# Kernel tuning notes

Hardware: AMD Instinct MI355X
Metric: run time of the kernel (lower is better)

The kernel has to match this reference:

```python
import jax, jax.numpy as jnp
import numpy as np

B, C, H, W = 16, 32, 240, 240  # C=32 forced: C//2 must equal 16 pooled-query tokens
CH = C // 2


def conv1x1(x, Wt, bt):
    # 1x1 conv == per-pixel matmul over channels
    return jnp.einsum('bchw,oc->bohw', x, Wt) + bt[None, :, None, None]


def adaptive_pool6(x):
    # AdaptiveAvgPool2d((6,6)) with H,W divisible by 6 -> uniform block mean
    b, c, h, w = x.shape
    return x.reshape(b, c, 6, h // 6, 6, w // 6).mean(axis=(3, 5))


def setup_inputs() -> dict:
    key = jax.random.key(0)
    ks = jax.random.split(key, 24)
    wsc, bsc = 0.05, 0.01
    def wmat(k, o, i):
        return jax.random.normal(k, (o, i), jnp.float32) * wsc
    def bvec(k, o):
        return jax.random.normal(k, (o,), jnp.float32) * bsc
    inp = {
        'x1': jax.random.normal(ks[0], (B, C, H, W), jnp.float32),
        'x2': jax.random.normal(ks[1], (B, C, H, W), jnp.float32),
        'Wq1': wmat(ks[2], CH, C), 'bq1': bvec(ks[3], CH),
        'Wk1': wmat(ks[4], CH, C), 'bk1': bvec(ks[5], CH),
        'Wv1': wmat(ks[6], CH, C), 'bv1': bvec(ks[7], CH),
        'Wq2': wmat(ks[8], CH, C), 'bq2': bvec(ks[9], CH),
        'Wk2': wmat(ks[10], CH, C), 'bk2': bvec(ks[11], CH),
        'Wv2': wmat(ks[12], CH, C), 'bv2': bvec(ks[13], CH),
        'Wc1': wmat(ks[14], C, CH), 'bc1': bvec(ks[15], C),
        'Wc2': wmat(ks[16], C, CH), 'bc2': bvec(ks[17], C),
        # module inits gammas to 0; use small nonzero so the attention path affects output
        'gamma1': jnp.float32(0.1),
        'gamma2': jnp.float32(0.1),
    }
    return inp


def reference(x1, x2, Wq1, bq1, Wk1, bk1, Wv1, bv1, Wq2, bq2, Wk2, bk2,
              Wv2, bv2, Wc1, bc1, Wc2, bc2, gamma1, gamma2):
    b, c, h, w = x1.shape
    hw = h * w
    ch = c // 2
    # pooled queries: 6x6 adaptive pool, crop interior 4x4 -> 16 tokens
    q1 = adaptive_pool6(conv1x1(x1, Wq1, bq1))[:, :, 1:-1, 1:-1]
    q1 = q1.reshape(b, ch, 16).transpose(0, 2, 1)          # [B,16,ch]
    k1 = conv1x1(x1, Wk1, bk1).reshape(b, ch, hw)           # [B,ch,HW]
    v1 = conv1x1(x1, Wv1, bv1).reshape(b, ch, hw)
    q2 = adaptive_pool6(conv1x1(x2, Wq2, bq2))[:, :, 1:-1, 1:-1]
    q2 = q2.reshape(b, ch, 16).transpose(0, 2, 1)
    k2 = conv1x1(x2, Wk2, bk2).reshape(b, ch, hw)
    v2 = conv1x1(x2, Wv2, bv2).reshape(b, ch, hw)

    attn2 = jax.nn.softmax(jnp.einsum('bqc,bcn->bqn', q1, k2), axis=-1)  # [B,16,HW]
    out1 = (v1 * attn2).reshape(b, ch, h, w)   # elementwise (ch == 16)
    out1 = conv1x1(out1, Wc2, bc2)

    attn1 = jax.nn.softmax(jnp.einsum('bqc,bcn->bqn', q2, k1), axis=-1)
    out2 = (v2 * attn1).reshape(b, ch, h, w)
    out2 = conv1x1(out2, Wc1, bc1)

    return (x1 + gamma1 * out1, x2 + gamma2 * out2)
```

## Files before the change

kernel.cpp:

```cpp
#include <hip/hip_runtime.h>

#define HW 57600
#define BATCH 16

#define L_OFF    0
#define AT_OFF   512
#define CV_OFF   16896
#define XM_OFF   17408
#define WVT_OFF  33792

__global__ void k1a_pool(const float* __restrict__ x1, const float* __restrict__ x2,
                         float* __restrict__ ws) {
  int task = blockIdx.x * 4 + (threadIdx.x >> 6);
  int lane = threadIdx.x & 63;
  int t = task & 15, i = (task >> 4) & 31, b = (task >> 9) & 15, s = task >> 13;
  int bi = 1 + (t >> 2), bj = 1 + (t & 3);
  const float* xp = (s ? x2 : x1) + (size_t)(b * 32 + i) * HW + (40 * bi) * 240 + 40 * bj;
  float sum = 0.f;
  #pragma unroll
  for (int k = 0; k < 25; ++k) {
    int e = lane + 64 * k;
    int r = e / 40, c = e - r * 40;
    sum += xp[r * 240 + c];
  }
  #pragma unroll
  for (int off = 32; off; off >>= 1) sum += __shfl_down(sum, off);
  if (lane == 0) ws[XM_OFF + task] = sum * (1.0f / 1600.0f);
}

__global__ void k1b_fold(float* __restrict__ ws,
                         const float* __restrict__ Wq1, const float* __restrict__ bq1,
                         const float* __restrict__ Wq2, const float* __restrict__ bq2,
                         const float* __restrict__ Wk1, const float* __restrict__ bk1,
                         const float* __restrict__ Wk2, const float* __restrict__ bk2,
                         const float* __restrict__ Wv1, const float* __restrict__ Wv2) {
  int s = blockIdx.x >> 4, b = blockIdx.x & 15;
  const float* Wq = s ? Wq2 : Wq1;
  const float* bq = s ? bq2 : bq1;
  const float* Wk = s ? Wk1 : Wk2;
  const float* bk = s ? bk1 : bk2;
  __shared__ float xm[32][16];
  __shared__ float qv[16][16];
  int tid = threadIdx.x;
  for (int e = tid; e < 512; e += 256)
    xm[e >> 4][e & 15] = ws[XM_OFF + (s * 16 + b) * 512 + e];
  __syncthreads();
  {
    int t = tid >> 4, c = tid & 15;
    float acc = bq[c];
    #pragma unroll
    for (int i = 0; i < 32; ++i) acc += Wq[c * 32 + i] * xm[i][t];
    qv[t][c] = acc;
  }
  __syncthreads();
  for (int e = tid; e < 512; e += 256) {
    int i = e >> 4, t = e & 15;
    float acc = 0.f;
    #pragma unroll
    for (int c = 0; c < 16; ++c) acc += qv[t][c] * Wk[c * 32 + i];
    ws[AT_OFF + (s * 16 + b) * 512 + i * 16 + t] = acc;
  }
  if (tid < 16) {
    float acc = 0.f;
    #pragma unroll
    for (int c = 0; c < 16; ++c) acc += qv[tid][c] * bk[c];
    ws[CV_OFF + (s * 16 + b) * 16 + tid] = acc;
  }
  if (b == 0) {
    const float* Wv = s ? Wv2 : Wv1;
    for (int e = tid; e < 512; e += 256) {
      int i = e >> 4, t = e & 15;
      ws[WVT_OFF + s * 512 + i * 16 + t] = Wv[t * 32 + i];
    }
  }
}

__global__ void k2_sumexp(const float* __restrict__ x1, const float* __restrict__ x2,
                          float* __restrict__ ws) {
  int slice = blockIdx.x >> 4;
  int sub = blockIdx.x & 15;
  int s = slice >> 4, b = slice & 15;
  const float* At = ws + AT_OFF + slice * 512;
  const float* cv = ws + CV_OFF + slice * 16;
  const float* xo = (s ? x1 : x2) + (size_t)b * 32 * HW;
  float* Lp = ws + L_OFF + slice * 16;
  float La[16];
  #pragma unroll
  for (int t = 0; t < 16; ++t) La[t] = 0.f;
  for (int n = sub * 256 + (int)threadIdx.x; n < HW; n += 4096) {
    float sc[16];
    #pragma unroll
    for (int t = 0; t < 16; ++t) sc[t] = cv[t];
    #pragma unroll
    for (int i = 0; i < 32; ++i) {
      float xi = xo[(size_t)i * HW + n];
      #pragma unroll
      for (int t = 0; t < 16; ++t) sc[t] += At[i * 16 + t] * xi;
    }
    #pragma unroll
    for (int t = 0; t < 16; ++t) La[t] += __expf(sc[t]);
  }
  #pragma unroll
  for (int t = 0; t < 16; ++t) {
    float v = La[t];
    #pragma unroll
    for (int off = 32; off; off >>= 1) v += __shfl_down(v, off);
    if ((threadIdx.x & 63) == 0) atomicAdd(&Lp[t], v);
  }
}

__global__ void k2b_log(float* __restrict__ ws) {
  int e = threadIdx.x;
  float L = ws[L_OFF + e];
  ws[CV_OFF + e] -= __logf(L);
}

__global__ void k3_out(const float* __restrict__ x1, const float* __restrict__ x2,
                       const float* __restrict__ ws,
                       const float* __restrict__ Wc1, const float* __restrict__ bc1,
                       const float* __restrict__ Wc2, const float* __restrict__ bc2,
                       const float* __restrict__ bv1, const float* __restrict__ bv2,
                       const float* __restrict__ g1p, const float* __restrict__ g2p,
                       float* __restrict__ out) {
  int b = blockIdx.x / 225;
  int n = (blockIdx.x % 225) * 256 + threadIdx.x;
  const float* At1 = ws + AT_OFF + b * 512;
  const float* At2 = ws + AT_OFF + 8192 + b * 512;
  const float* cv1 = ws + CV_OFF + b * 16;
  const float* cv2 = ws + CV_OFF + 256 + b * 16;
  const float* Wv1T = ws + WVT_OFF;
  const float* Wv2T = ws + WVT_OFF + 512;
  float g1 = g1p[0], g2 = g2p[0];
  const float* x1b = x1 + (size_t)b * 32 * HW + n;
  const float* x2b = x2 + (size_t)b * 32 * HW + n;
  float xa[32], xb[32];
  #pragma unroll
  for (int i = 0; i < 32; ++i) xa[i] = x1b[(size_t)i * HW];
  #pragma unroll
  for (int i = 0; i < 32; ++i) xb[i] = x2b[(size_t)i * HW];

  float sc[16], vv[16], o16[16];
  #pragma unroll
  for (int t = 0; t < 16; ++t) { sc[t] = cv1[t]; vv[t] = bv1[t]; }
  #pragma unroll
  for (int i = 0; i < 32; ++i) {
    float a = xa[i], bx = xb[i];
    #pragma unroll
    for (int t = 0; t < 16; ++t) {
      sc[t] += At1[i * 16 + t] * bx;
      vv[t] += Wv1T[i * 16 + t] * a;
    }
  }
  #pragma unroll
  for (int t = 0; t < 16; ++t) o16[t] = vv[t] * __expf(sc[t]);
  float* out1 = out + (size_t)b * 32 * HW + n;
  #pragma unroll
  for (int o = 0; o < 32; ++o) {
    float acc = bc2[o];
    #pragma unroll
    for (int t = 0; t < 16; ++t) acc += Wc2[o * 16 + t] * o16[t];
    out1[(size_t)o * HW] = xa[o] + g1 * acc;
  }
  #pragma unroll
  for (int t = 0; t < 16; ++t) { sc[t] = cv2[t]; vv[t] = bv2[t]; }
  #pragma unroll
  for (int i = 0; i < 32; ++i) {
    float a = xa[i], bx = xb[i];
    #pragma unroll
    for (int t = 0; t < 16; ++t) {
      sc[t] += At2[i * 16 + t] * a;
      vv[t] += Wv2T[i * 16 + t] * bx;
    }
  }
  #pragma unroll
  for (int t = 0; t < 16; ++t) o16[t] = vv[t] * __expf(sc[t]);
  float* out2 = out + (size_t)(BATCH * 32) * HW + (size_t)b * 32 * HW + n;
  #pragma unroll
  for (int o = 0; o < 32; ++o) {
    float acc = bc1[o];
    #pragma unroll
    for (int t = 0; t < 16; ++t) acc += Wc1[o * 16 + t] * o16[t];
    out2[(size_t)o * HW] = xb[o] + g2 * acc;
  }
}

extern "C" void kernel_launch(void* const* d_in, const int* in_sizes, int n_in,
                              void* d_out, int out_size, void* d_ws, size_t ws_size,
                              hipStream_t stream) {
  const float* x1  = (const float*)d_in[0];
  const float* x2  = (const float*)d_in[1];
  const float* Wq1 = (const float*)d_in[2];  const float* bq1 = (const float*)d_in[3];
  const float* Wk1 = (const float*)d_in[4];  const float* bk1 = (const float*)d_in[5];
  const float* Wv1 = (const float*)d_in[6];  const float* bv1 = (const float*)d_in[7];
  const float* Wq2 = (const float*)d_in[8];  const float* bq2 = (const float*)d_in[9];
  const float* Wk2 = (const float*)d_in[10]; const float* bk2 = (const float*)d_in[11];
  const float* Wv2 = (const float*)d_in[12]; const float* bv2 = (const float*)d_in[13];
  const float* Wc1 = (const float*)d_in[14]; const float* bc1 = (const float*)d_in[15];
  const float* Wc2 = (const float*)d_in[16]; const float* bc2 = (const float*)d_in[17];
  const float* g1  = (const float*)d_in[18]; const float* g2  = (const float*)d_in[19];
  float* out = (float*)d_out;
  float* ws  = (float*)d_ws;

  hipMemsetAsync(d_ws, 0, 512 * sizeof(float), stream);
  k1a_pool<<<4096, 256, 0, stream>>>(x1, x2, ws);
  k1b_fold<<<32, 256, 0, stream>>>(ws, Wq1, bq1, Wq2, bq2, Wk1, bk1, Wk2, bk2, Wv1, Wv2);
  k2_sumexp<<<512, 256, 0, stream>>>(x1, x2, ws);
  k2b_log<<<1, 512, 0, stream>>>(ws);
  k3_out<<<3600, 256, 0, stream>>>(x1, x2, ws, Wc1, bc1, Wc2, bc2, bv1, bv2, g1, g2, out);
}
```

Measured before the change: 754.1 us.

## Vectorize sumexp with float4 pixels and restructure output kernel to cut register pressure

```diff
diff --git a/kernel.cpp b/kernel.cpp
--- a/kernel.cpp
+++ b/kernel.cpp
@@ -77,28 +77,39 @@
 
 __global__ void k2_sumexp(const float* __restrict__ x1, const float* __restrict__ x2,
                           float* __restrict__ ws) {
-  int slice = blockIdx.x >> 4;
-  int sub = blockIdx.x & 15;
+  int slice = blockIdx.x / 57;
+  int blk = blockIdx.x % 57;
   int s = slice >> 4, b = slice & 15;
-  const float* At = ws + AT_OFF + slice * 512;
-  const float* cv = ws + CV_OFF + slice * 16;
-  const float* xo = (s ? x1 : x2) + (size_t)b * 32 * HW;
+  const float* __restrict__ At = ws + AT_OFF + slice * 512;
+  const float* __restrict__ cv = ws + CV_OFF + slice * 16;
+  const float4* __restrict__ xo4 =
+      (const float4*)((s ? x1 : x2) + (size_t)b * 32 * HW);
   float* Lp = ws + L_OFF + slice * 16;
+
+  int q = blk * 256 + (int)threadIdx.x;
   float La[16];
   #pragma unroll
   for (int t = 0; t < 16; ++t) La[t] = 0.f;
-  for (int n = sub * 256 + (int)threadIdx.x; n < HW; n += 4096) {
-    float sc[16];
-    #pragma unroll
-    for (int t = 0; t < 16; ++t) sc[t] = cv[t];
-    #pragma unroll
+
+  if (q < HW / 4) {
+    float sc0[16], sc1[16], sc2[16], sc3[16];
+    #pragma unroll
+    for (int t = 0; t < 16; ++t) { float c = cv[t]; sc0[t] = c; sc1[t] = c; sc2[t] = c; sc3[t] = c; }
+    #pragma unroll 4
     for (int i = 0; i < 32; ++i) {
-      float xi = xo[(size_t)i * HW + n];
+      float4 xi = xo4[(size_t)i * (HW / 4) + q];
       #pragma unroll
-      for (int t = 0; t < 16; ++t) sc[t] += At[i * 16 + t] * xi;
-    }
-    #pragma unroll
-    for (int t = 0; t < 16; ++t) La[t] += __expf(sc[t]);
+      for (int t = 0; t < 16; ++t) {
+        float w = At[i * 16 + t];
+        sc0[t] += w * xi.x;
+        sc1[t] += w * xi.y;
+        sc2[t] += w * xi.z;
+        sc3[t] += w * xi.w;
+      }
+    }
+    #pragma unroll
+    for (int t = 0; t < 16; ++t)
+      La[t] = __expf(sc0[t]) + __expf(sc1[t]) + __expf(sc2[t]) + __expf(sc3[t]);
   }
   #pragma unroll
   for (int t = 0; t < 16; ++t) {
@@ -124,63 +135,53 @@
                        float* __restrict__ out) {
   int b = blockIdx.x / 225;
   int n = (blockIdx.x % 225) * 256 + threadIdx.x;
-  const float* At1 = ws + AT_OFF + b * 512;
-  const float* At2 = ws + AT_OFF + 8192 + b * 512;
-  const float* cv1 = ws + CV_OFF + b * 16;
-  const float* cv2 = ws + CV_OFF + 256 + b * 16;
-  const float* Wv1T = ws + WVT_OFF;
-  const float* Wv2T = ws + WVT_OFF + 512;
+  const float* __restrict__ At1 = ws + AT_OFF + b * 512;
+  const float* __restrict__ At2 = ws + AT_OFF + 8192 + b * 512;
+  const float* __restrict__ cv1 = ws + CV_OFF + b * 16;
+  const float* __restrict__ cv2 = ws + CV_OFF + 256 + b * 16;
+  const float* __restrict__ Wv1T = ws + WVT_OFF;
+  const float* __restrict__ Wv2T = ws + WVT_OFF + 512;
   float g1 = g1p[0], g2 = g2p[0];
   const float* x1b = x1 + (size_t)b * 32 * HW + n;
   const float* x2b = x2 + (size_t)b * 32 * HW + n;
-  float xa[32], xb[32];
-  #pragma unroll
-  for (int i = 0; i < 32; ++i) xa[i] = x1b[(size_t)i * HW];
-  #pragma unroll
-  for (int i = 0; i < 32; ++i) xb[i] = x2b[(size_t)i * HW];
-
-  float sc[16], vv[16], o16[16];
-  #pragma unroll
-  for (int t = 0; t < 16; ++t) { sc[t] = cv1[t]; vv[t] = bv1[t]; }
-  #pragma unroll
+
+  float sc1[16], vv1[16], sc2[16], vv2[16];
+  #pragma unroll
+  for (int t = 0; t < 16; ++t) {
+    sc1[t] = cv1[t]; vv1[t] = bv1[t];
+    sc2[t] = cv2[t]; vv2[t] = bv2[t];
+  }
+  #pragma unroll 8
   for (int i = 0; i < 32; ++i) {
-    float a = xa[i], bx = xb[i];
+    float a = x1b[(size_t)i * HW];
+    float bx = x2b[(size_t)i * HW];
     #pragma unroll
     for (int t = 0; t < 16; ++t) {
-      sc[t] += At1[i * 16 + t] * bx;
-      vv[t] += Wv1T[i * 16 + t] * a;
-    }
-  }
-  #pragma unroll
-  for (int t = 0; t < 16; ++t) o16[t] = vv[t] * __expf(sc[t]);
+      sc1[t] += At1[i * 16 + t] * bx;
+      vv1[t] += Wv1T[i * 16 + t] * a;
+      sc2[t] += At2[i * 16 + t] * a;
+      vv2[t] += Wv2T[i * 16 + t] * bx;
+    }
+  }
+  #pragma unroll
+  for (int t = 0; t < 16; ++t) {
+    sc1[t] = vv1[t] * __expf(sc1[t]);
+    sc2[t] = vv2[t] * __expf(sc2[t]);
+  }
   float* out1 = out + (size_t)b * 32 * HW + n;
-  #pragma unroll
+  float* out2 = out + (size_t)(BATCH * 32) * HW + (size_t)b * 32 * HW + n;
+  #pragma unroll 8
   for (int o = 0; o < 32; ++o) {
-    float acc = bc2[o];
-    #pragma unroll
-    for (int t = 0; t < 16; ++t) acc += Wc2[o * 16 + t] * o16[t];
-    out1[(size_t)o * HW] = xa[o] + g1 * acc;
-  }
-  #pragma unroll
-  for (int t = 0; t < 16; ++t) { sc[t] = cv2[t]; vv[t] = bv2[t]; }
-  #pragma unroll
-  for (int i = 0; i < 32; ++i) {
-    float a = xa[i], bx = xb[i];
+    float acc1 = bc2[o], acc2 = bc1[o];
     #pragma unroll
     for (int t = 0; t < 16; ++t) {
-      sc[t] += At2[i * 16 + t] * a;
-      vv[t] += Wv2T[i * 16 + t] * bx;
-    }
-  }
-  #pragma unroll
-  for (int t = 0; t < 16; ++t) o16[t] = vv[t] * __expf(sc[t]);
-  float* out2 = out + (size_t)(BATCH * 32) * HW + (size_t)b * 32 * HW + n;
-  #pragma unroll
-  for (int o = 0; o < 32; ++o) {
-    float acc = bc1[o];
-    #pragma unroll
-    for (int t = 0; t < 16; ++t) acc += Wc1[o * 16 + t] * o16[t];
-    out2[(size_t)o * HW] = xb[o] + g2 * acc;
+      acc1 += Wc2[o * 16 + t] * sc1[t];
+      acc2 += Wc1[o * 16 + t] * sc2[t];
+    }
+    float xa = x1b[(size_t)o * HW];
+    float xb = x2b[(size_t)o * HW];
+    out1[(size_t)o * HW] = xa + g1 * acc1;
+    out2[(size_t)o * HW] = xb + g2 * acc2;
   }
 }
 
@@ -204,7 +205,7 @@
   hipMemsetAsync(d_ws, 0, 512 * sizeof(float), stream);
   k1a_pool<<<4096, 256, 0, stream>>>(x1, x2, ws);
   k1b_fold<<<32, 256, 0, stream>>>(ws, Wq1, bq1, Wq2, bq2, Wk1, bk1, Wk2, bk2, Wv1, Wv2);
-  k2_sumexp<<<512, 256, 0, stream>>>(x1, x2, ws);
+  k2_sumexp<<<32 * 57, 256, 0, stream>>>(x1, x2, ws);
   k2b_log<<<1, 512, 0, stream>>>(ws);
   k3_out<<<3600, 256, 0, stream>>>(x1, x2, ws, Wc1, bc1, Wc2, bc2, bv1, bv2, g1, g2, out);
 }
```

New measurement: 789.5 us. 1.05x slower.
